# Kernel optimization log

Measured on AMD Instinct MI355X. Metric: run time of the kernel, lower is better.

The kernel has to match this reference:

```python
import jax, jax.numpy as jnp
import numpy as np


def setup_inputs() -> dict:
    key = jax.random.key(0)
    heatmaps = jax.random.normal(key, (16, 24, 64, 64, 64), dtype=jnp.float32)
    return {"heatmaps": heatmaps}


def reference(heatmaps):
    N, J, D, H, W = heatmaps.shape
    # Softmax over the flattened D*H*W volume (the intended normalization).
    p = jax.nn.softmax(heatmaps.reshape(N, J, D * H * W), axis=-1)
    p = p.reshape(N, J, D, H, W)
    # Axis marginals: sum out the other two spatial axes.
    x_maps = p.sum(axis=(2, 3))  # [N, J, W]
    y_maps = p.sum(axis=(2, 4))  # [N, J, H]
    z_maps = p.sum(axis=(3, 4))  # [N, J, D]
    # Soft-argmax expectation, normalized to roughly [-0.5, 0.5).
    x_preds = (x_maps * jnp.arange(W, dtype=p.dtype)).sum(axis=2) / W - 0.5
    y_preds = (y_maps * jnp.arange(H, dtype=p.dtype)).sum(axis=2) / H - 0.5
    z_preds = (z_maps * jnp.arange(D, dtype=p.dtype)).sum(axis=2) / D - 0.5
    return jnp.stack((x_preds, y_preds, z_preds), axis=2)  # [N, J, 3]
```

## Files before the change

### kernel.cpp

```cpp
#include <hip/hip_runtime.h>
#include <math.h>


#define SLABS       384
#define SLAB_ELEMS  262144
#define CHUNKS      8
#define BLOCK       256
#define CHUNK_ELEMS (SLAB_ELEMS / CHUNKS)
#define ITERS       (CHUNK_ELEMS / (BLOCK * 8))

typedef float f32x4 __attribute__((ext_vector_type(4)));

__device__ __forceinline__ float fast_exp2(float x) {
#if __has_builtin(__builtin_amdgcn_exp2f)
    return __builtin_amdgcn_exp2f(x);
#else
    return exp2f(x);
#endif
}

__global__ __launch_bounds__(BLOCK) void jir_partial_kernel(const float* __restrict__ in,
                                                            float* __restrict__ ws) {
    const int slab  = blockIdx.x / CHUNKS;
    const int chunk = blockIdx.x % CHUNKS;
    const f32x4* __restrict__ B =
        (const f32x4*)(in + (size_t)slab * SLAB_ELEMS + (size_t)chunk * CHUNK_ELEMS);
    const int tid = threadIdx.x;

    const float LOG2E = 1.4426950408889634f;

    const float w0f   = (float)((4 * tid) & 63);
    const float hbase = (float)(tid >> 4);
    const float dbase = (float)(chunk * 8);

    float S = 0.f, Sx = 0.f, Sy = 0.f, Sz = 0.f;

#pragma unroll
    for (int it = 0; it < ITERS; ++it) {
        const f32x4 va = B[it * (2 * BLOCK) + tid];
        const f32x4 vb = B[it * (2 * BLOCK) + BLOCK + tid];

        const float h0f = hbase + (float)((it & 1) << 5);
        const float ddf = dbase + (float)(it >> 1);

        const float a0 = fast_exp2(va.x * LOG2E);
        const float a1 = fast_exp2(va.y * LOG2E);
        const float a2 = fast_exp2(va.z * LOG2E);
        const float a3 = fast_exp2(va.w * LOG2E);
        const float b0 = fast_exp2(vb.x * LOG2E);
        const float b1 = fast_exp2(vb.y * LOG2E);
        const float b2 = fast_exp2(vb.z * LOG2E);
        const float b3 = fast_exp2(vb.w * LOG2E);

        const float sA = (a0 + a1) + (a2 + a3);
        const float sB = (b0 + b1) + (b2 + b3);
        const float xA = __builtin_fmaf(3.f, a3, __builtin_fmaf(2.f, a2, a1));
        const float xB = __builtin_fmaf(3.f, b3, __builtin_fmaf(2.f, b2, b1));
        const float sAB = sA + sB;

        S  += sAB;
        Sx  = __builtin_fmaf(sAB, w0f, Sx + (xA + xB));
        Sy  = __builtin_fmaf(sAB, h0f, __builtin_fmaf(16.f, sB, Sy));
        Sz  = __builtin_fmaf(sAB, ddf, Sz);
    }

#pragma unroll
    for (int off = 1; off < 64; off <<= 1) {
        S  += __shfl_xor(S,  off, 64);
        Sx += __shfl_xor(Sx, off, 64);
        Sy += __shfl_xor(Sy, off, 64);
        Sz += __shfl_xor(Sz, off, 64);
    }

    __shared__ float red[4][4];
    const int wave = tid >> 6;
    const int lane = tid & 63;
    if (lane == 0) {
        red[wave][0] = S; red[wave][1] = Sx; red[wave][2] = Sy; red[wave][3] = Sz;
    }
    __syncthreads();
    if (tid == 0) {
        float fS  = red[0][0] + red[1][0] + red[2][0] + red[3][0];
        float fSx = red[0][1] + red[1][1] + red[2][1] + red[3][1];
        float fSy = red[0][2] + red[1][2] + red[2][2] + red[3][2];
        float fSz = red[0][3] + red[1][3] + red[2][3] + red[3][3];
        float* o = ws + (size_t)blockIdx.x * 4;
        o[0] = fS; o[1] = fSx; o[2] = fSy; o[3] = fSz;
    }
}

__global__ __launch_bounds__(64) void jir_finalize_kernel(const float* __restrict__ ws,
                                                          float* __restrict__ out) {
    const int slab = blockIdx.x * 64 + threadIdx.x;
    if (slab >= SLABS) return;

    const float* p0 = ws + (size_t)slab * CHUNKS * 4;
    float S = 0.f, Sx = 0.f, Sy = 0.f, Sz = 0.f;
#pragma unroll
    for (int c = 0; c < CHUNKS; ++c) {
        const float* p = p0 + c * 4;
        S += p[0]; Sx += p[1]; Sy += p[2]; Sz += p[3];
    }
    const float inv = 1.0f / S;
    out[slab * 3 + 0] = (Sx * inv) * (1.0f / 64.0f) - 0.5f;
    out[slab * 3 + 1] = (Sy * inv) * (1.0f / 64.0f) - 0.5f;
    out[slab * 3 + 2] = (Sz * inv) * (1.0f / 64.0f) - 0.5f;
}

extern "C" void kernel_launch(void* const* d_in, const int* in_sizes, int n_in,
                              void* d_out, int out_size, void* d_ws, size_t ws_size,
                              hipStream_t stream) {
    const float* heatmaps = (const float*)d_in[0];
    float* out = (float*)d_out;
    float* ws = (float*)d_ws;

    jir_partial_kernel<<<SLABS * CHUNKS, BLOCK, 0, stream>>>(heatmaps, ws);
    jir_finalize_kernel<<<(SLABS + 63) / 64, 64, 0, stream>>>(ws, out);
}
```

Before: 513.3 us.

## Grid-stride blocks across slabs with per-iteration wave partials to workspace

Each block now walks the whole input with a grid-sized stride and handles one 2048-element row segment per iteration, so concurrently running blocks read adjacent memory. Each wave reduces every iteration's partial sums with shuffles and writes a float4 to the workspace, which removes the LDS reduction and __syncthreads. The finalize kernel now uses one wave per slab to sum 512 partials. The cost is a wave shuffle reduction in every iteration, which is extra ALU and cross-lane work in a kernel that is memory-bound, plus more workspace traffic.

```diff
diff --git a/kernel.cpp b/kernel.cpp
--- a/kernel.cpp
+++ b/kernel.cpp
@@ -4,10 +4,9 @@
 
 #define SLABS       384
 #define SLAB_ELEMS  262144
-#define CHUNKS      8
 #define BLOCK       256
-#define CHUNK_ELEMS (SLAB_ELEMS / CHUNKS)
-#define ITERS       (CHUNK_ELEMS / (BLOCK * 8))
+#define GRID        3072
+#define ITERS       16
 
 typedef float f32x4 __attribute__((ext_vector_type(4)));
 
@@ -21,27 +20,24 @@
 
 __global__ __launch_bounds__(BLOCK) void jir_partial_kernel(const float* __restrict__ in,
                                                             float* __restrict__ ws) {
-    const int slab  = blockIdx.x / CHUNKS;
-    const int chunk = blockIdx.x % CHUNKS;
-    const f32x4* __restrict__ B =
-        (const f32x4*)(in + (size_t)slab * SLAB_ELEMS + (size_t)chunk * CHUNK_ELEMS);
-    const int tid = threadIdx.x;
+    const int b    = blockIdx.x;
+    const int t    = threadIdx.x;
+    const int wv   = t >> 6;
+    const int lane = t & 63;
 
     const float LOG2E = 1.4426950408889634f;
 
-    const float w0f   = (float)((4 * tid) & 63);
-    const float hbase = (float)(tid >> 4);
-    const float dbase = (float)(chunk * 8);
+    const float w0f = (float)((4 * t) & 63);
+    const float hf  = (float)(((b & 1) << 5) + (t >> 4));
+    const float df  = (float)((b & 127) >> 1);
 
-    float S = 0.f, Sx = 0.f, Sy = 0.f, Sz = 0.f;
+    const f32x4* __restrict__ base = (const f32x4*)in + (size_t)b * 512 + t;
+    f32x4* __restrict__ wbase = (f32x4*)ws + (size_t)b * 4 + wv;
 
-#pragma unroll
-    for (int it = 0; it < ITERS; ++it) {
-        const f32x4 va = B[it * (2 * BLOCK) + tid];
-        const f32x4 vb = B[it * (2 * BLOCK) + BLOCK + tid];
-
-        const float h0f = hbase + (float)((it & 1) << 5);
-        const float ddf = dbase + (float)(it >> 1);
+#pragma unroll 4
+    for (int i = 0; i < ITERS; ++i) {
+        const f32x4 va = base[(size_t)i * (GRID * 512)];
+        const f32x4 vb = base[(size_t)i * (GRID * 512) + 256];
 
         const float a0 = fast_exp2(va.x * LOG2E);
         const float a1 = fast_exp2(va.y * LOG2E);
@@ -56,14 +52,40 @@
         const float sB = (b0 + b1) + (b2 + b3);
         const float xA = __builtin_fmaf(3.f, a3, __builtin_fmaf(2.f, a2, a1));
         const float xB = __builtin_fmaf(3.f, b3, __builtin_fmaf(2.f, b2, b1));
-        const float sAB = sA + sB;
+        const float s  = sA + sB;
 
-        S  += sAB;
-        Sx  = __builtin_fmaf(sAB, w0f, Sx + (xA + xB));
-        Sy  = __builtin_fmaf(sAB, h0f, __builtin_fmaf(16.f, sB, Sy));
-        Sz  = __builtin_fmaf(sAB, ddf, Sz);
+        float S  = s;
+        float Sx = __builtin_fmaf(s, w0f, xA + xB);
+        float Sy = __builtin_fmaf(s, hf, 16.f * sB);
+        float Sz = df * s;
+
+#pragma unroll
+        for (int off = 1; off < 64; off <<= 1) {
+            S  += __shfl_xor(S,  off, 64);
+            Sx += __shfl_xor(Sx, off, 64);
+            Sy += __shfl_xor(Sy, off, 64);
+            Sz += __shfl_xor(Sz, off, 64);
+        }
+
+        if (lane == 0) {
+            f32x4 o; o.x = S; o.y = Sx; o.z = Sy; o.w = Sz;
+            wbase[(size_t)i * (GRID * 4)] = o;
+        }
     }
+}
 
+__global__ __launch_bounds__(64) void jir_finalize_kernel(const float* __restrict__ ws,
+                                                          float* __restrict__ out) {
+    const int s    = blockIdx.x;
+    const int lane = threadIdx.x;
+
+    const f32x4* __restrict__ p = (const f32x4*)ws + (size_t)s * 512 + lane;
+    float S = 0.f, Sx = 0.f, Sy = 0.f, Sz = 0.f;
+#pragma unroll
+    for (int k = 0; k < 8; ++k) {
+        const f32x4 v = p[k * 64];
+        S += v.x; Sx += v.y; Sy += v.z; Sz += v.w;
+    }
 #pragma unroll
     for (int off = 1; off < 64; off <<= 1) {
         S  += __shfl_xor(S,  off, 64);
@@ -71,40 +93,12 @@
         Sy += __shfl_xor(Sy, off, 64);
         Sz += __shfl_xor(Sz, off, 64);
     }
-
-    __shared__ float red[4][4];
-    const int wave = tid >> 6;
-    const int lane = tid & 63;
     if (lane == 0) {
-        red[wave][0] = S; red[wave][1] = Sx; red[wave][2] = Sy; red[wave][3] = Sz;
+        const float inv = 1.0f / S;
+        out[s * 3 + 0] = (Sx * inv) * (1.0f / 64.0f) - 0.5f;
+        out[s * 3 + 1] = (Sy * inv) * (1.0f / 64.0f) - 0.5f;
+        out[s * 3 + 2] = (Sz * inv) * (1.0f / 64.0f) - 0.5f;
     }
-    __syncthreads();
-    if (tid == 0) {
-        float fS  = red[0][0] + red[1][0] + red[2][0] + red[3][0];
-        float fSx = red[0][1] + red[1][1] + red[2][1] + red[3][1];
-        float fSy = red[0][2] + red[1][2] + red[2][2] + red[3][2];
-        float fSz = red[0][3] + red[1][3] + red[2][3] + red[3][3];
-        float* o = ws + (size_t)blockIdx.x * 4;
-        o[0] = fS; o[1] = fSx; o[2] = fSy; o[3] = fSz;
-    }
-}
-
-__global__ __launch_bounds__(64) void jir_finalize_kernel(const float* __restrict__ ws,
-                                                          float* __restrict__ out) {
-    const int slab = blockIdx.x * 64 + threadIdx.x;
-    if (slab >= SLABS) return;
-
-    const float* p0 = ws + (size_t)slab * CHUNKS * 4;
-    float S = 0.f, Sx = 0.f, Sy = 0.f, Sz = 0.f;
-#pragma unroll
-    for (int c = 0; c < CHUNKS; ++c) {
-        const float* p = p0 + c * 4;
-        S += p[0]; Sx += p[1]; Sy += p[2]; Sz += p[3];
-    }
-    const float inv = 1.0f / S;
-    out[slab * 3 + 0] = (Sx * inv) * (1.0f / 64.0f) - 0.5f;
-    out[slab * 3 + 1] = (Sy * inv) * (1.0f / 64.0f) - 0.5f;
-    out[slab * 3 + 2] = (Sz * inv) * (1.0f / 64.0f) - 0.5f;
 }
 
 extern "C" void kernel_launch(void* const* d_in, const int* in_sizes, int n_in,
@@ -114,6 +108,6 @@
     float* out = (float*)d_out;
     float* ws = (float*)d_ws;
 
-    jir_partial_kernel<<<SLABS * CHUNKS, BLOCK, 0, stream>>>(heatmaps, ws);
-    jir_finalize_kernel<<<(SLABS + 63) / 64, 64, 0, stream>>>(ws, out);
+    jir_partial_kernel<<<GRID, BLOCK, 0, stream>>>(heatmaps, ws);
+    jir_finalize_kernel<<<SLABS, 64, 0, stream>>>(ws, out);
 }
```

New measurement: 525.5 us. +2.4%, slower.
